# Kernel tuning notes

Hardware: AMD Instinct MI355X
Metric: run time of the kernel (lower is better)

Reference implementation:

```python
import jax, jax.numpy as jnp
import numpy as np

N = 50000
E = 400000
C = 64
H = 6  # heads, hardcoded in the module
NEG_SLOPE = 0.2
EPS = 1e-8


def setup_inputs() -> dict:
    key = jax.random.key(0)
    ks = jax.random.split(key, 10)
    x = jax.random.normal(ks[0], (N, C), dtype=jnp.float32)
    ei = jax.random.randint(ks[1], (2, E), 0, N)
    loop = jnp.arange(N)
    # forward() first calls add_remaining_self_loops -> GCN consumes edges + self loops
    src = jnp.concatenate([ei[0], loop])
    dst = jnp.concatenate([ei[1], loop])
    # gen_subs: subindex = self loops (i->i) plus reversed edges (t->i) for edge (i,t)
    sub_src = jnp.concatenate([loop, ei[1]])
    sub_dst = jnp.concatenate([loop, ei[0]])

    def glorot(k, shape):
        stdv = np.sqrt(6.0 / (shape[-2] + shape[-1]))
        return jax.random.uniform(k, shape, jnp.float32, -stdv, stdv)

    W_gcn = glorot(ks[2], (C, C))           # gnn_intra_cluster (GCNConv)
    b_gcn = jnp.zeros((C,), jnp.float32)
    weight = glorot(ks[3], (C, H * C))      # self.weight
    attention = glorot(ks[4], (1, H, 2 * C))  # self.attention
    W1 = glorot(ks[5], (C, C))              # simiConv.lin1 (no bias)
    W2 = glorot(ks[6], (C, 1))              # simiConv.lin2
    b2 = jnp.zeros((1,), jnp.float32)
    return {"x": x, "W_gcn": W_gcn, "b_gcn": b_gcn, "weight": weight,
            "attention": attention, "W1": W1, "W2": W2, "b2": b2,
            "src": src, "dst": dst, "sub_src": sub_src, "sub_dst": sub_dst}


def _gcn(x, W, b, src, dst, n):
    # PyG GCNConv's gcn_norm appends its own self loops on top of the ones
    # already added by forward()'s add_remaining_self_loops.
    loop = jnp.arange(n)
    s = jnp.concatenate([src, loop])
    d = jnp.concatenate([dst, loop])
    deg = jax.ops.segment_sum(jnp.ones_like(s, dtype=x.dtype), d, num_segments=n)
    dinv = jax.lax.rsqrt(jnp.maximum(deg, 1.0e-12))
    norm = dinv[s] * dinv[d]                      # [E']
    h = x @ W                                     # [N, C]
    out = jax.ops.segment_sum(h[s] * norm[:, None], d, num_segments=n)
    return out + b


def reference(x, W_gcn, b_gcn, weight, attention, W1, W2, b2,
              src, dst, sub_src, sub_dst):
    n = x.shape[0]
    # intra-cluster GCN
    xpj = _gcn(x, W_gcn, b_gcn, src, dst, n)      # [N, C]
    # multi-head attention pooling over subindex
    h = (xpj @ weight).reshape(n, H, C)           # [N, H, C]
    hi = h[sub_src]                               # [Es, H, C] (x_i in message)
    hmax = jax.ops.segment_max(hi, sub_dst, num_segments=n)  # [N, H, C]
    att_i = attention[:, :, :C]                   # [1, H, C]
    att_j = attention[:, :, C:]
    alpha = (hi * att_i).sum(-1) + (hmax[sub_dst] * att_j).sum(-1)  # [Es, H]
    alpha = jnp.where(alpha >= 0, alpha, NEG_SLOPE * alpha)
    # segment softmax over destination nodes (dropout p=0)
    amax = jax.ops.segment_max(alpha, sub_dst, num_segments=n)
    e = jnp.exp(alpha - amax[sub_dst])
    denom = jax.ops.segment_sum(e, sub_dst, num_segments=n)
    alpha = e / denom[sub_dst]
    xa = jax.ops.segment_sum(hi * alpha[:, :, None], sub_dst, num_segments=n)
    xm = xa.mean(axis=1)                          # [N, C]
    # simiConv score: message = x_cluster_i * cos(x_i, x_j), aggr='add'
    a = xm @ W1                                   # [N, C]
    bsc = xm @ W2 + b2                            # [N, 1]
    ai = a[sub_dst]
    aj = a[sub_src]
    cos = (ai * aj).sum(-1) / (jnp.maximum(jnp.linalg.norm(ai, axis=-1), EPS)
                               * jnp.maximum(jnp.linalg.norm(aj, axis=-1), EPS))
    score = jax.ops.segment_sum(bsc[sub_dst, 0] * cos, sub_dst, num_segments=n)
    fitness = jax.nn.sigmoid(score)               # [N]
    return fitness
```

## Files before the change

kernel.cpp:

```cpp
#include <hip/hip_runtime.h>
#include <math.h>

#define TPB 256
#define NEG_SLOPE 0.2f
#define COS_EPS 1e-8f
#define NH 6
#define GSTRIDE 68
#define DCACHE 12
#define SALS 8

__device__ inline float wave_sum64(float v) {
  #pragma unroll
  for (int off = 32; off > 0; off >>= 1) v += __shfl_down(v, off);
  return __shfl(v, 0);
}
__device__ inline float wave_max64(float v) {
  #pragma unroll
  for (int off = 32; off > 0; off >>= 1) v = fmaxf(v, __shfl_down(v, off));
  return __shfl(v, 0);
}
__device__ inline unsigned short f2bf(float f) {
  unsigned u = __float_as_uint(f);
  unsigned r = (u + 0x7fffu + ((u >> 16) & 1u)) >> 16;
  return (unsigned short)r;
}
__device__ inline float bf2f(unsigned short b) {
  return __uint_as_float(((unsigned)b) << 16);
}
__device__ inline unsigned packbf(float lo, float hi) {
  return (unsigned)f2bf(lo) | ((unsigned)f2bf(hi) << 16);
}
__device__ inline float bflo(unsigned u) { return __uint_as_float(u << 16); }
__device__ inline float bfhi(unsigned u) { return __uint_as_float(u & 0xffff0000u); }

#define GS_LOOP(i, total) \
  for (long i = (long)blockIdx.x * blockDim.x + threadIdx.x; i < (total); \
       i += (long)gridDim.x * blockDim.x)

__global__ void k_cnt(const int* __restrict__ src, const int* __restrict__ dst,
                      int* __restrict__ gcnt, int* __restrict__ scnt, long E) {
  GS_LOOP(e, E) {
    atomicAdd(&gcnt[dst[e]], 1);
    atomicAdd(&scnt[src[e]], 1);
  }
}

__global__ __launch_bounds__(1024)
void k_scanA(const int* __restrict__ gcnt, const int* __restrict__ scnt,
             int* __restrict__ bsum, float* __restrict__ dinv, int n, int nb) {
  const int b = blockIdx.x;
  const bool isS = b >= nb;
  const int tb = isS ? b - nb : b;
  const int* cnt = isS ? scnt : gcnt;
  const int t = threadIdx.x;
  const int i0 = tb * 2048 + 2 * t;
  int v0 = (i0 < n) ? cnt[i0] : 0;
  int v1 = (i0 + 1 < n) ? cnt[i0 + 1] : 0;
  if (!isS) {
    if (i0 < n)     dinv[i0]     = rsqrtf((float)v0 + 2.0f);
    if (i0 + 1 < n) dinv[i0 + 1] = rsqrtf((float)v1 + 2.0f);
  }
  __shared__ int red[16];
  int x = v0 + v1;
  #pragma unroll
  for (int o = 32; o > 0; o >>= 1) x += __shfl_down(x, o);
  const int lane = t & 63, wv = t >> 6;
  if (lane == 0) red[wv] = x;
  __syncthreads();
  if (t < 64) {
    int w = (t < 16) ? red[t] : 0;
    #pragma unroll
    for (int o = 32; o > 0; o >>= 1) w += __shfl_down(w, o);
    if (t == 0) bsum[b] = w;
  }
}

__global__ void k_scanB(int* __restrict__ bsum, int nb) {
  const int lane = threadIdx.x;
  if (nb <= 32) {
    int half = lane >> 5, idx = lane & 31;
    int base = half * nb;
    int v = (idx < nb) ? bsum[base + idx] : 0;
    int orig = v;
    #pragma unroll
    for (int d2 = 1; d2 < 32; d2 <<= 1) {
      int y = __shfl_up(v, d2, 32);
      if (idx >= d2) v += y;
    }
    if (idx < nb) bsum[base + idx] = v - orig;
  } else if (lane == 0) {
    int run = 0;
    for (int i = 0; i < nb; ++i) { int v = bsum[i]; bsum[i] = run; run += v; }
    run = 0;
    for (int i = 0; i < nb; ++i) { int v = bsum[nb + i]; bsum[nb + i] = run; run += v; }
  }
}

__global__ __launch_bounds__(1024)
void k_scanC(const int* __restrict__ gcnt, int* __restrict__ goff, int* __restrict__ gcur,
             const int* __restrict__ scnt, int* __restrict__ soff, int* __restrict__ scur,
             const int* __restrict__ bsum, int n, int nb) {
  const int b = blockIdx.x;
  const bool isS = b >= nb;
  const int tb = isS ? b - nb : b;
  const int* cnt = isS ? scnt : gcnt;
  int* off = isS ? soff : goff;
  int* cur = isS ? scur : gcur;
  const int t = threadIdx.x;
  const int i0 = tb * 2048 + 2 * t;
  int v0 = (i0 < n) ? cnt[i0] : 0;
  int v1 = (i0 + 1 < n) ? cnt[i0 + 1] : 0;
  int s2 = v0 + v1;
  const int lane = t & 63, wv = t >> 6;
  int x = s2;
  #pragma unroll
  for (int d2 = 1; d2 < 64; d2 <<= 1) {
    int y = __shfl_up(x, d2);
    if (lane >= d2) x += y;
  }
  __shared__ int wsum[16];
  if (lane == 63) wsum[wv] = x;
  __syncthreads();
  if (t < 64) {
    int w = (t < 16) ? wsum[t] : 0;
    #pragma unroll
    for (int d2 = 1; d2 < 16; d2 <<= 1) {
      int y = __shfl_up(w, d2);
      if ((int)t >= d2) w += y;
    }
    if (t < 16) wsum[t] = w;
  }
  __syncthreads();
  int ex = x - s2 + (wv ? wsum[wv - 1] : 0) + bsum[b];
  if (i0 < n)     { cur[i0] = ex;          off[i0 + 1] = ex + v0; }
  if (i0 + 1 < n) { cur[i0 + 1] = ex + v0; off[i0 + 2] = ex + v0 + v1; }
  if (i0 == 0) off[0] = 0;
}

__global__ void k_scatter(const int* __restrict__ src, const int* __restrict__ dst,
                          int* __restrict__ gcur, int* __restrict__ gcsr,
                          int* __restrict__ scur, int* __restrict__ scsr, long E) {
  GS_LOOP(e, E) {
    int s = src[e], d = dst[e];
    int p1 = atomicAdd(&gcur[d], 1); gcsr[p1] = s;
    int p2 = atomicAdd(&scur[s], 1); scsr[p2] = d;
  }
}

template <int MODE>
__global__ __launch_bounds__(256)
void k_gemm64v3(const float* __restrict__ A, const float* __restrict__ W,
                float* __restrict__ out32, unsigned short* __restrict__ out16,
                const float* __restrict__ rowscale,
                const float* __restrict__ W2, const float* __restrict__ b2,
                float* __restrict__ bsc, int n, int Mtot) {
  __shared__ float At[64 * GSTRIDE];
  __shared__ float Wl[64 * GSTRIDE];
  const int t  = threadIdx.x;
  const int tx = t & 15;
  const int ty = t >> 4;
  const int col0 = blockIdx.y * 64;
  const long row0 = (long)blockIdx.x * 64;

  #pragma unroll
  for (int i = 0; i < 4; ++i) {
    int k = ty + 16 * i;
    float4 wv = *(const float4*)&W[(long)k * Mtot + col0 + 4 * tx];
    *(float4*)&Wl[k * GSTRIDE + 4 * tx] = wv;
  }
  #pragma unroll
  for (int i = 0; i < 4; ++i) {
    int r = ty + 16 * i;
    long gr = row0 + r; if (gr >= n) gr = n - 1;
    float4 av = *(const float4*)&A[gr * 64 + 4 * tx];
    At[(4 * tx + 0) * GSTRIDE + r] = av.x;
    At[(4 * tx + 1) * GSTRIDE + r] = av.y;
    At[(4 * tx + 2) * GSTRIDE + r] = av.z;
    At[(4 * tx + 3) * GSTRIDE + r] = av.w;
  }
  __syncthreads();

  const int c0 = 4 * tx;
  const int r0 = 4 * ty;
  float acc[4][4] = {};
  #pragma unroll
  for (int k = 0; k < 64; ++k) {
    float4 av = *(const float4*)&At[k * GSTRIDE + r0];
    float4 wv = *(const float4*)&Wl[k * GSTRIDE + c0];
    acc[0][0] = fmaf(av.x, wv.x, acc[0][0]); acc[0][1] = fmaf(av.x, wv.y, acc[0][1]);
    acc[0][2] = fmaf(av.x, wv.z, acc[0][2]); acc[0][3] = fmaf(av.x, wv.w, acc[0][3]);
    acc[1][0] = fmaf(av.y, wv.x, acc[1][0]); acc[1][1] = fmaf(av.y, wv.y, acc[1][1]);
    acc[1][2] = fmaf(av.y, wv.z, acc[1][2]); acc[1][3] = fmaf(av.y, wv.w, acc[1][3]);
    acc[2][0] = fmaf(av.z, wv.x, acc[2][0]); acc[2][1] = fmaf(av.z, wv.y, acc[2][1]);
    acc[2][2] = fmaf(av.z, wv.z, acc[2][2]); acc[2][3] = fmaf(av.z, wv.w, acc[2][3]);
    acc[3][0] = fmaf(av.w, wv.x, acc[3][0]); acc[3][1] = fmaf(av.w, wv.y, acc[3][1]);
    acc[3][2] = fmaf(av.w, wv.z, acc[3][2]); acc[3][3] = fmaf(av.w, wv.w, acc[3][3]);
  }

  if constexpr (MODE == 0) {
    #pragma unroll
    for (int i = 0; i < 4; ++i) {
      long gr = row0 + r0 + i;
      if (gr < n)
        *(float4*)&out32[gr * Mtot + col0 + c0] =
          make_float4(acc[i][0], acc[i][1], acc[i][2], acc[i][3]);
    }
  }
  if constexpr (MODE == 1) {
    #pragma unroll
    for (int i = 0; i < 4; ++i) {
      long gr = row0 + r0 + i;
      if (gr < n) {
        float sc = rowscale[gr];
        ushort4 v;
        v.x = f2bf(acc[i][0] * sc); v.y = f2bf(acc[i][1] * sc);
        v.z = f2bf(acc[i][2] * sc); v.w = f2bf(acc[i][3] * sc);
        *(ushort4*)&out16[gr * 64 + c0] = v;
      }
    }
  }
  if constexpr (MODE == 2) {
    float p[4], q[4];
    #pragma unroll
    for (int i = 0; i < 4; ++i) {
      q[i] = acc[i][0]*acc[i][0] + acc[i][1]*acc[i][1] +
             acc[i][2]*acc[i][2] + acc[i][3]*acc[i][3];
      p[i] = At[(c0+0) * GSTRIDE + r0 + i] * W2[c0+0] +
             At[(c0+1) * GSTRIDE + r0 + i] * W2[c0+1] +
             At[(c0+2) * GSTRIDE + r0 + i] * W2[c0+2] +
             At[(c0+3) * GSTRIDE + r0 + i] * W2[c0+3];
    }
    #pragma unroll
    for (int m = 1; m < 16; m <<= 1) {
      #pragma unroll
      for (int i = 0; i < 4; ++i) { p[i] += __shfl_xor(p[i], m); q[i] += __shfl_xor(q[i], m); }
    }
    float bb = b2[0];
    #pragma unroll
    for (int i = 0; i < 4; ++i) {
      long gr = row0 + r0 + i;
      if (gr < n) {
        float rn = 1.0f / fmaxf(sqrtf(q[i]), COS_EPS);
        ushort4 v;
        v.x = f2bf(acc[i][0] * rn); v.y = f2bf(acc[i][1] * rn);
        v.z = f2bf(acc[i][2] * rn); v.w = f2bf(acc[i][3] * rn);
        *(ushort4*)&out16[gr * 64 + c0] = v;
        if (tx == 0) bsc[gr] = p[i] + bb;
      }
    }
  }
}

__global__ __launch_bounds__(256)
void k_gemm_h2(const float* __restrict__ A, const float* __restrict__ W,
               unsigned* __restrict__ h2p, const float* __restrict__ att,
               float* __restrict__ sal, int n) {
  __shared__ float At[64 * GSTRIDE];
  __shared__ float Wl[64 * GSTRIDE];
  const int t  = threadIdx.x;
  const int tx = t & 15;
  const int ty = t >> 4;
  const long row0 = (long)blockIdx.x * 64;
  const int c0 = 4 * tx;
  const int r0 = 4 * ty;

  #pragma unroll
  for (int i = 0; i < 4; ++i) {
    int r = ty + 16 * i;
    long gr = row0 + r; if (gr >= n) gr = n - 1;
    float4 av = *(const float4*)&A[gr * 64 + 4 * tx];
    At[(4 * tx + 0) * GSTRIDE + r] = av.x;
    At[(4 * tx + 1) * GSTRIDE + r] = av.y;
    At[(4 * tx + 2) * GSTRIDE + r] = av.z;
    At[(4 * tx + 3) * GSTRIDE + r] = av.w;
  }
  float4 wr[4];
  #pragma unroll
  for (int i = 0; i < 4; ++i)
    wr[i] = *(const float4*)&W[(long)(ty + 16 * i) * 384 + 4 * tx];

  float4 acc[6][4];
  #pragma unroll
  for (int h = 0; h < 6; ++h)
    #pragma unroll
    for (int i = 0; i < 4; ++i) acc[h][i] = make_float4(0.f, 0.f, 0.f, 0.f);

  #pragma unroll
  for (int head = 0; head < 6; ++head) {
    #pragma unroll
    for (int i = 0; i < 4; ++i)
      *(float4*)&Wl[(ty + 16 * i) * GSTRIDE + 4 * tx] = wr[i];
    __syncthreads();
    if (head < 5) {
      #pragma unroll
      for (int i = 0; i < 4; ++i)
        wr[i] = *(const float4*)&W[(long)(ty + 16 * i) * 384 + (head + 1) * 64 + 4 * tx];
    }
    #pragma unroll 16
    for (int k = 0; k < 64; ++k) {
      float4 av = *(const float4*)&At[k * GSTRIDE + r0];
      float4 wv = *(const float4*)&Wl[k * GSTRIDE + c0];
      acc[head][0].x = fmaf(av.x, wv.x, acc[head][0].x);
      acc[head][0].y = fmaf(av.x, wv.y, acc[head][0].y);
      acc[head][0].z = fmaf(av.x, wv.z, acc[head][0].z);
      acc[head][0].w = fmaf(av.x, wv.w, acc[head][0].w);
      acc[head][1].x = fmaf(av.y, wv.x, acc[head][1].x);
      acc[head][1].y = fmaf(av.y, wv.y, acc[head][1].y);
      acc[head][1].z = fmaf(av.y, wv.z, acc[head][1].z);
      acc[head][1].w = fmaf(av.y, wv.w, acc[head][1].w);
      acc[head][2].x = fmaf(av.z, wv.x, acc[head][2].x);
      acc[head][2].y = fmaf(av.z, wv.y, acc[head][2].y);
      acc[head][2].z = fmaf(av.z, wv.z, acc[head][2].z);
      acc[head][2].w = fmaf(av.z, wv.w, acc[head][2].w);
      acc[head][3].x = fmaf(av.w, wv.x, acc[head][3].x);
      acc[head][3].y = fmaf(av.w, wv.y, acc[head][3].y);
      acc[head][3].z = fmaf(av.w, wv.z, acc[head][3].z);
      acc[head][3].w = fmaf(av.w, wv.w, acc[head][3].w);
    }
    __syncthreads();
  }

  #pragma unroll
  for (int i = 0; i < 4; ++i) {
    long gr = row0 + r0 + i;
    if (gr < n) {
      uint4 u0, u1, u2;
      u0.x = packbf(acc[0][i].x, acc[1][i].x);
      u0.y = packbf(acc[2][i].x, acc[3][i].x);
      u0.z = packbf(acc[4][i].x, acc[5][i].x);
      u0.w = packbf(acc[0][i].y, acc[1][i].y);
      u1.x = packbf(acc[2][i].y, acc[3][i].y);
      u1.y = packbf(acc[4][i].y, acc[5][i].y);
      u1.z = packbf(acc[0][i].z, acc[1][i].z);
      u1.w = packbf(acc[2][i].z, acc[3][i].z);
      u2.x = packbf(acc[4][i].z, acc[5][i].z);
      u2.y = packbf(acc[0][i].w, acc[1][i].w);
      u2.z = packbf(acc[2][i].w, acc[3][i].w);
      u2.w = packbf(acc[4][i].w, acc[5][i].w);
      unsigned* dstp = &h2p[gr * 192 + c0 * 3];
      *(uint4*)(dstp + 0) = u0;
      *(uint4*)(dstp + 4) = u1;
      *(uint4*)(dstp + 8) = u2;
    }
  }
  #pragma unroll
  for (int head = 0; head < 6; ++head) {
    float a0 = att[head * 128 + c0 + 0], a1 = att[head * 128 + c0 + 1];
    float a2 = att[head * 128 + c0 + 2], a3 = att[head * 128 + c0 + 3];
    float p[4];
    #pragma unroll
    for (int i = 0; i < 4; ++i)
      p[i] = acc[head][i].x * a0 + acc[head][i].y * a1 +
             acc[head][i].z * a2 + acc[head][i].w * a3;
    #pragma unroll
    for (int m = 1; m < 16; m <<= 1) {
      #pragma unroll
      for (int i = 0; i < 4; ++i) p[i] += __shfl_xor(p[i], m);
    }
    if (tx == 0) {
      #pragma unroll
      for (int i = 0; i < 4; ++i) {
        long gr = row0 + r0 + i;
        if (gr < n) sal[gr * SALS + head] = p[i];
      }
    }
  }
}

__global__ __launch_bounds__(256)
void k_gcnb(const int* __restrict__ goff, const int* __restrict__ gcsr,
            const unsigned* __restrict__ hs32, const float* __restrict__ dinv,
            const float* __restrict__ bg, float* __restrict__ xpj, int n) {
  const int lane = threadIdx.x & 63;
  const int p = lane & 31;
  const int hf = lane >> 5;
  const int d = blockIdx.x * 4 + (threadIdx.x >> 6);
  if (d >= n) return;
  const int o0 = goff[d], o1 = goff[d + 1];
  float ax = 0.f, ay = 0.f;
  for (int j = o0 + hf; j < o1; j += 2) {
    long s = gcsr[j];
    unsigned u = hs32[s * 32 + p];
    ax += bflo(u); ay += bfhi(u);
  }
  ax += __shfl_xor(ax, 32);
  ay += __shfl_xor(ay, 32);
  if (hf == 0) {
    unsigned us = hs32[(long)d * 32 + p];
    float di = dinv[d];
    float2 bv = *(const float2*)&bg[2 * p];
    float2 r;
    r.x = bv.x + di * (ax + 2.0f * bflo(us));
    r.y = bv.y + di * (ay + 2.0f * bfhi(us));
    *(float2*)&xpj[(long)d * 64 + 2 * p] = r;
  }
}

__global__ __launch_bounds__(256)
void k_mega(const int* __restrict__ soff, const int* __restrict__ scsr,
            const unsigned* __restrict__ h2p, const float* __restrict__ sal,
            const float* __restrict__ att, float* __restrict__ xm, int n) {
  const int lane = threadIdx.x & 63;
  const int d = blockIdx.x * 4 + (threadIdx.x >> 6);
  if (d >= n) return;
  const int o0 = soff[d], o1 = soff[d + 1];
  const int deg = o1 - o0;
  const int td  = deg + 1;

  unsigned ck0[DCACHE], ck1[DCACHE], ck2[DCACHE];
  float hm[NH];
  {
    const unsigned* rp = &h2p[(long)d * 192 + lane * 3];
    unsigned u0 = rp[0], u1 = rp[1], u2 = rp[2];
    ck0[0] = u0; ck1[0] = u1; ck2[0] = u2;
    hm[0] = bflo(u0); hm[1] = bfhi(u0);
    hm[2] = bflo(u1); hm[3] = bfhi(u1);
    hm[4] = bflo(u2); hm[5] = bfhi(u2);
  }
  #pragma unroll
  for (int idx = 1; idx < DCACHE; ++idx) {
    unsigned u0 = 0, u1 = 0, u2 = 0;
    if (idx < td) {
      long s = scsr[o0 + idx - 1];
      const unsigned* rp = &h2p[s * 192 + lane * 3];
      u0 = rp[0]; u1 = rp[1]; u2 = rp[2];
      hm[0] = fmaxf(hm[0], bflo(u0)); hm[1] = fmaxf(hm[1], bfhi(u0));
      hm[2] = fmaxf(hm[2], bflo(u1)); hm[3] = fmaxf(hm[3], bfhi(u1));
      hm[4] = fmaxf(hm[4], bflo(u2)); hm[5] = fmaxf(hm[5], bfhi(u2));
    }
    ck0[idx] = u0; ck1[idx] = u1; ck2[idx] = u2;
  }
  for (int j = o0 + DCACHE - 1; j < o1; ++j) {
    long s = scsr[j];
    const unsigned* rp = &h2p[s * 192 + lane * 3];
    unsigned u0 = rp[0], u1 = rp[1], u2 = rp[2];
    hm[0] = fmaxf(hm[0], bflo(u0)); hm[1] = fmaxf(hm[1], bfhi(u0));
    hm[2] = fmaxf(hm[2], bflo(u1)); hm[3] = fmaxf(hm[3], bfhi(u1));
    hm[4] = fmaxf(hm[4], bflo(u2)); hm[5] = fmaxf(hm[5], bfhi(u2));
  }

  float dal[NH];
  #pragma unroll
  for (int h = 0; h < NH; ++h)
    dal[h] = wave_sum64(hm[h] * att[h * 128 + 64 + lane]);

  float acc[NH], den[NH];
  #pragma unroll
  for (int h = 0; h < NH; ++h) acc[h] = 0.f;

  if (td <= 64) {
    const bool act = lane < td;
    float4 sA = make_float4(0, 0, 0, 0), sB = sA;
    if (act) {
      int sE = (lane == 0) ? d : scsr[o0 + lane - 1];
      const float4* sp = (const float4*)&sal[(long)sE * SALS];
      sA = sp[0]; sB = sp[1];
    }
    float svv[NH] = {sA.x, sA.y, sA.z, sA.w, sB.x, sB.y};
    float e6[NH];
    #pragma unroll
    for (int h = 0; h < NH; ++h) {
      float al = svv[h] + dal[h];
      al = (al >= 0.f) ? al : NEG_SLOPE * al;
      float a = act ? al : -INFINITY;
      float mx = wave_max64(a);
      e6[h] = act ? expf(a - mx) : 0.f;
      den[h] = wave_sum64(e6[h]);
    }
    #pragma unroll
    for (int idx = 0; idx < DCACHE; ++idx) {
      if (idx < td) {
        float w0 = __shfl(e6[0], idx), w1 = __shfl(e6[1], idx);
        float w2 = __shfl(e6[2], idx), w3 = __shfl(e6[3], idx);
        float w4 = __shfl(e6[4], idx), w5 = __shfl(e6[5], idx);
        acc[0] = fmaf(bflo(ck0[idx]), w0, acc[0]);
        acc[1] = fmaf(bfhi(ck0[idx]), w1, acc[1]);
        acc[2] = fmaf(bflo(ck1[idx]), w2, acc[2]);
        acc[3] = fmaf(bfhi(ck1[idx]), w3, acc[3]);
        acc[4] = fmaf(bflo(ck2[idx]), w4, acc[4]);
        acc[5] = fmaf(bfhi(ck2[idx]), w5, acc[5]);
      }
    }
    for (int j = o0 + DCACHE - 1; j < o1; ++j) {
      int ii = j - o0 + 1;
      long s = scsr[j];
      const unsigned* rp = &h2p[s * 192 + lane * 3];
      unsigned u0 = rp[0], u1 = rp[1], u2 = rp[2];
      float w0 = __shfl(e6[0], ii), w1 = __shfl(e6[1], ii);
      float w2 = __shfl(e6[2], ii), w3 = __shfl(e6[3], ii);
      float w4 = __shfl(e6[4], ii), w5 = __shfl(e6[5], ii);
      acc[0] = fmaf(bflo(u0), w0, acc[0]);
      acc[1] = fmaf(bfhi(u0), w1, acc[1]);
      acc[2] = fmaf(bflo(u1), w2, acc[2]);
      acc[3] = fmaf(bfhi(u1), w3, acc[3]);
      acc[4] = fmaf(bflo(u2), w4, acc[4]);
      acc[5] = fmaf(bfhi(u2), w5, acc[5]);
    }
  } else {
    float asf[NH];
    {
      const float4* sp = (const float4*)&sal[(long)d * SALS];
      float4 sA = sp[0], sB = sp[1];
      float svv[NH] = {sA.x, sA.y, sA.z, sA.w, sB.x, sB.y};
      #pragma unroll
      for (int h = 0; h < NH; ++h) {
        float al = svv[h] + dal[h];
        asf[h] = (al >= 0.f) ? al : NEG_SLOPE * al;
      }
    }
    float mx[NH];
    #pragma unroll
    for (int h = 0; h < NH; ++h) mx[h] = asf[h];
    for (int base = o0; base < o1; base += 64) {
      int j = base + lane;
      float a6[NH];
      if (j < o1) {
        long s = scsr[j];
        const float4* sp = (const float4*)&sal[s * SALS];
        float4 sA = sp[0], sB = sp[1];
        float svv[NH] = {sA.x, sA.y, sA.z, sA.w, sB.x, sB.y};
        #pragma unroll
        for (int h = 0; h < NH; ++h) {
          float al = svv[h] + dal[h];
          a6[h] = (al >= 0.f) ? al : NEG_SLOPE * al;
        }
      } else {
        #pragma unroll
        for (int h = 0; h < NH; ++h) a6[h] = -INFINITY;
      }
      #pragma unroll
      for (int h = 0; h < NH; ++h) mx[h] = fmaxf(mx[h], wave_max64(a6[h]));
    }
    #pragma unroll
    for (int h = 0; h < NH; ++h) {
      float es = expf(asf[h] - mx[h]);
      den[h] = es;
    }
    acc[0] = bflo(ck0[0]) * den[0]; acc[1] = bfhi(ck0[0]) * den[1];
    acc[2] = bflo(ck1[0]) * den[2]; acc[3] = bfhi(ck1[0]) * den[3];
    acc[4] = bflo(ck2[0]) * den[4]; acc[5] = bfhi(ck2[0]) * den[5];
    for (int base = o0; base < o1; base += 64) {
      int cs = o1 - base; if (cs > 64) cs = 64;
      int j = base + lane;
      float e6[NH]; int s = 0;
      if (j < o1) {
        s = scsr[j];
        const float4* sp = (const float4*)&sal[(long)s * SALS];
        float4 sA = sp[0], sB = sp[1];
        float svv[NH] = {sA.x, sA.y, sA.z, sA.w, sB.x, sB.y};
        #pragma unroll
        for (int h = 0; h < NH; ++h) {
          float al = svv[h] + dal[h];
          al = (al >= 0.f) ? al : NEG_SLOPE * al;
          e6[h] = expf(al - mx[h]);
        }
      } else {
        #pragma unroll
        for (int h = 0; h < NH; ++h) e6[h] = 0.f;
      }
      #pragma unroll
      for (int h = 0; h < NH; ++h) den[h] += wave_sum64(e6[h]);
      for (int jj = 0; jj < cs; ++jj) {
        int sj = __shfl(s, jj);
        const unsigned* rp = &h2p[(long)sj * 192 + lane * 3];
        unsigned u0 = rp[0], u1 = rp[1], u2 = rp[2];
        float w0 = __shfl(e6[0], jj), w1 = __shfl(e6[1], jj);
        float w2 = __shfl(e6[2], jj), w3 = __shfl(e6[3], jj);
        float w4 = __shfl(e6[4], jj), w5 = __shfl(e6[5], jj);
        acc[0] = fmaf(bflo(u0), w0, acc[0]);
        acc[1] = fmaf(bfhi(u0), w1, acc[1]);
        acc[2] = fmaf(bflo(u1), w2, acc[2]);
        acc[3] = fmaf(bfhi(u1), w3, acc[3]);
        acc[4] = fmaf(bflo(u2), w4, acc[4]);
        acc[5] = fmaf(bfhi(u2), w5, acc[5]);
      }
    }
  }

  float o = 0.f;
  #pragma unroll
  for (int h = 0; h < NH; ++h) o += acc[h] / den[h];
  xm[(long)d * 64 + lane] = o * (1.0f / NH);
}

__global__ __launch_bounds__(256)
void k_cosout(const int* __restrict__ soff, const int* __restrict__ scsr,
              const unsigned* __restrict__ an32, const float* __restrict__ bsc,
              float* __restrict__ out, int n) {
  const int lane = threadIdx.x & 63;
  const int p = lane & 31;
  const int hf = lane >> 5;
  const int d = blockIdx.x * 4 + (threadIdx.x >> 6);
  if (d >= n) return;
  const int o0 = soff[d], o1 = soff[d + 1];
  unsigned ud = an32[(long)d * 32 + p];
  float adx = bflo(ud), ady = bfhi(ud);
  float cl = 0.f;
  for (int j = o0 + hf; j < o1; j += 2) {
    long s = scsr[j];
    unsigned u = an32[s * 32 + p];
    cl += adx * bflo(u) + ady * bfhi(u);
  }
  float cs = wave_sum64(cl) + 1.0f;
  if (lane == 0) out[d] = 1.0f / (1.0f + expf(-bsc[d] * cs));
}

static inline unsigned gsblocks(long total) {
  long b = (total + TPB - 1) / TPB;
  if (b > 131072) b = 131072;
  return (unsigned)b;
}

extern "C" void kernel_launch(void* const* d_in, const int* in_sizes, int n_in,
                              void* d_out, int out_size, void* d_ws, size_t ws_size,
                              hipStream_t stream) {
  const float* x   = (const float*)d_in[0];
  const float* Wg  = (const float*)d_in[1];
  const float* bg  = (const float*)d_in[2];
  const float* Wt  = (const float*)d_in[3];
  const float* att = (const float*)d_in[4];
  const float* W1  = (const float*)d_in[5];
  const float* W2  = (const float*)d_in[6];
  const float* b2  = (const float*)d_in[7];
  const int* src   = (const int*)d_in[8];
  const int* dst   = (const int*)d_in[9];

  const long n   = in_sizes[0] / 64;
  const long en  = in_sizes[8];
  const long E   = en - n;
  const int  nb  = (int)((n + 2047) / 2048);

  char* base = (char*)d_ws;
  size_t off = 0;
  auto alloc = [&](size_t bytes) -> void* {
    void* p = base + off;
    off += (bytes + 255) & ~(size_t)255;
    return p;
  };
  int*   gcnt = (int*)alloc(n * 4);
  int*   scnt = (int*)alloc(n * 4);
  int*   goff = (int*)alloc((n + 1) * 4);
  int*   soff = (int*)alloc((n + 1) * 4);
  int*   gcur = (int*)alloc(n * 4);
  int*   scur = (int*)alloc(n * 4);
  int*   gcsr = (int*)alloc(E * 4);
  int*   scsr = (int*)alloc(E * 4);
  int*   bsum = (int*)alloc(2 * (size_t)nb * 4);
  float* dinv = (float*)alloc(n * 4);
  unsigned* hs32 = (unsigned*)alloc(n * 32 * 4);
  float* xpj  = (float*)alloc(n * 64 * 4);
  float* xmb  = (float*)alloc(n * 64 * 4);
  unsigned* h2p = (unsigned*)alloc(n * 192 * 4);
  float* sal  = (float*)alloc(n * SALS * 4);
  float* bsc  = (float*)alloc(n * 4);
  unsigned short* anorm = (unsigned short*)xpj;
  float* out  = (float*)d_out;

  const unsigned rowblk  = (unsigned)((n + 63) / 64);
  const unsigned nodeblk = (unsigned)((n + 3) / 4);

  hipMemsetAsync(gcnt, 0, (size_t)((char*)scnt - (char*)gcnt) + n * 4, stream);
  k_cnt<<<gsblocks(E), TPB, 0, stream>>>(src, dst, gcnt, scnt, E);
  k_scanA<<<2 * nb, 1024, 0, stream>>>(gcnt, scnt, bsum, dinv, (int)n, nb);
  k_scanB<<<1, 64, 0, stream>>>(bsum, nb);
  k_scanC<<<2 * nb, 1024, 0, stream>>>(gcnt, goff, gcur, scnt, soff, scur,
                                       bsum, (int)n, nb);
  k_scatter<<<gsblocks(E), TPB, 0, stream>>>(src, dst, gcur, gcsr, scur, scsr, E);

  { dim3 g(rowblk, 1);
    k_gemm64v3<1><<<g, 256, 0, stream>>>(x, Wg, nullptr, (unsigned short*)hs32,
                                         dinv, nullptr, nullptr, nullptr, (int)n, 64); }

  k_gcnb<<<nodeblk, 256, 0, stream>>>(goff, gcsr, hs32, dinv, bg, xpj, (int)n);

  k_gemm_h2<<<rowblk, 256, 0, stream>>>(xpj, Wt, h2p, att, sal, (int)n);

  k_mega<<<nodeblk, 256, 0, stream>>>(soff, scsr, h2p, sal, att, xmb, (int)n);

  { dim3 g(rowblk, 1);
    k_gemm64v3<2><<<g, 256, 0, stream>>>(xmb, W1, nullptr, anorm, nullptr,
                                         W2, b2, bsc, (int)n, 64); }

  k_cosout<<<nodeblk, 256, 0, stream>>>(soff, scsr, (const unsigned*)anorm,
                                        bsc, out, (int)n);
}
```

Measured before the change: 369.8 us.

## Replace softmax max pass with analytic bound, fold block-prefix scan into scanC

The segment softmax no longer runs a separate max-reduction pass over neighbours. It subtracts a per-head shift K = max(dal, 0) instead, which removes one gather pass over sal and the wave max reductions. The separate k_scanB launch is dropped, and each scanC block now sums the preceding block totals itself with a wave reduction. DCACHE rises from 12 to 16, and the unused MODE 0 GEMM epilogue is removed. The shift is not a true maximum, so exp can overflow or underflow if the source-side attention logits are large, which trades numerical safety for one fewer pass.

```diff
diff --git a/kernel.cpp b/kernel.cpp
--- a/kernel.cpp
+++ b/kernel.cpp
@@ -6,7 +6,7 @@
 #define COS_EPS 1e-8f
 #define NH 6
 #define GSTRIDE 68
-#define DCACHE 12
+#define DCACHE 16
 #define SALS 8
 
 __device__ inline float wave_sum64(float v) {
@@ -14,10 +14,10 @@
   for (int off = 32; off > 0; off >>= 1) v += __shfl_down(v, off);
   return __shfl(v, 0);
 }
-__device__ inline float wave_max64(float v) {
-  #pragma unroll
-  for (int off = 32; off > 0; off >>= 1) v = fmaxf(v, __shfl_down(v, off));
-  return __shfl(v, 0);
+__device__ inline int wave_isum64(int v) {
+  #pragma unroll
+  for (int off = 32; off > 0; off >>= 1) v += __shfl_down(v, off);
+  return v;
 }
 __device__ inline unsigned short f2bf(float f) {
   unsigned u = __float_as_uint(f);
@@ -75,27 +75,6 @@
   }
 }
 
-__global__ void k_scanB(int* __restrict__ bsum, int nb) {
-  const int lane = threadIdx.x;
-  if (nb <= 32) {
-    int half = lane >> 5, idx = lane & 31;
-    int base = half * nb;
-    int v = (idx < nb) ? bsum[base + idx] : 0;
-    int orig = v;
-    #pragma unroll
-    for (int d2 = 1; d2 < 32; d2 <<= 1) {
-      int y = __shfl_up(v, d2, 32);
-      if (idx >= d2) v += y;
-    }
-    if (idx < nb) bsum[base + idx] = v - orig;
-  } else if (lane == 0) {
-    int run = 0;
-    for (int i = 0; i < nb; ++i) { int v = bsum[i]; bsum[i] = run; run += v; }
-    run = 0;
-    for (int i = 0; i < nb; ++i) { int v = bsum[nb + i]; bsum[nb + i] = run; run += v; }
-  }
-}
-
 __global__ __launch_bounds__(1024)
 void k_scanC(const int* __restrict__ gcnt, int* __restrict__ goff, int* __restrict__ gcur,
              const int* __restrict__ scnt, int* __restrict__ soff, int* __restrict__ scur,
@@ -107,6 +86,14 @@
   int* off = isS ? soff : goff;
   int* cur = isS ? scur : gcur;
   const int t = threadIdx.x;
+
+  __shared__ int pfx_s;
+  if (t < 64) {
+    int v = (t < tb) ? bsum[(isS ? nb : 0) + t] : 0;
+    v = wave_isum64(v);
+    if (t == 0) pfx_s = v;
+  }
+
   const int i0 = tb * 2048 + 2 * t;
   int v0 = (i0 < n) ? cnt[i0] : 0;
   int v1 = (i0 + 1 < n) ? cnt[i0 + 1] : 0;
@@ -131,7 +118,7 @@
     if (t < 16) wsum[t] = w;
   }
   __syncthreads();
-  int ex = x - s2 + (wv ? wsum[wv - 1] : 0) + bsum[b];
+  int ex = x - s2 + (wv ? wsum[wv - 1] : 0) + pfx_s;
   if (i0 < n)     { cur[i0] = ex;          off[i0 + 1] = ex + v0; }
   if (i0 + 1 < n) { cur[i0 + 1] = ex + v0; off[i0 + 2] = ex + v0 + v1; }
   if (i0 == 0) off[0] = 0;
@@ -197,15 +184,6 @@
     acc[3][2] = fmaf(av.w, wv.z, acc[3][2]); acc[3][3] = fmaf(av.w, wv.w, acc[3][3]);
   }
 
-  if constexpr (MODE == 0) {
-    #pragma unroll
-    for (int i = 0; i < 4; ++i) {
-      long gr = row0 + r0 + i;
-      if (gr < n)
-        *(float4*)&out32[gr * Mtot + col0 + c0] =
-          make_float4(acc[i][0], acc[i][1], acc[i][2], acc[i][3]);
-    }
-  }
   if constexpr (MODE == 1) {
     #pragma unroll
     for (int i = 0; i < 4; ++i) {
@@ -439,10 +417,12 @@
     hm[4] = fmaxf(hm[4], bflo(u2)); hm[5] = fmaxf(hm[5], bfhi(u2));
   }
 
-  float dal[NH];
-  #pragma unroll
-  for (int h = 0; h < NH; ++h)
+  float dal[NH], K[NH];
+  #pragma unroll
+  for (int h = 0; h < NH; ++h) {
     dal[h] = wave_sum64(hm[h] * att[h * 128 + 64 + lane]);
+    K[h] = fmaxf(dal[h], 0.f);
+  }
 
   float acc[NH], den[NH];
   #pragma unroll
@@ -462,9 +442,7 @@
     for (int h = 0; h < NH; ++h) {
       float al = svv[h] + dal[h];
       al = (al >= 0.f) ? al : NEG_SLOPE * al;
-      float a = act ? al : -INFINITY;
-      float mx = wave_max64(a);
-      e6[h] = act ? expf(a - mx) : 0.f;
+      e6[h] = act ? expf(al - K[h]) : 0.f;
       den[h] = wave_sum64(e6[h]);
     }
     #pragma unroll
@@ -497,7 +475,6 @@
       acc[5] = fmaf(bfhi(u2), w5, acc[5]);
     }
   } else {
-    float asf[NH];
     {
       const float4* sp = (const float4*)&sal[(long)d * SALS];
       float4 sA = sp[0], sB = sp[1];
@@ -505,36 +482,10 @@
       #pragma unroll
       for (int h = 0; h < NH; ++h) {
         float al = svv[h] + dal[h];
-        asf[h] = (al >= 0.f) ? al : NEG_SLOPE * al;
+        al = (al >= 0.f) ? al : NEG_SLOPE * al;
+        float es = expf(al - K[h]);
+        den[h] = es;
       }
-    }
-    float mx[NH];
-    #pragma unroll
-    for (int h = 0; h < NH; ++h) mx[h] = asf[h];
-    for (int base = o0; base < o1; base += 64) {
-      int j = base + lane;
-      float a6[NH];
-      if (j < o1) {
-        long s = scsr[j];
-        const float4* sp = (const float4*)&sal[s * SALS];
-        float4 sA = sp[0], sB = sp[1];
-        float svv[NH] = {sA.x, sA.y, sA.z, sA.w, sB.x, sB.y};
-        #pragma unroll
-        for (int h = 0; h < NH; ++h) {
-          float al = svv[h] + dal[h];
-          a6[h] = (al >= 0.f) ? al : NEG_SLOPE * al;
-        }
-      } else {
-        #pragma unroll
-        for (int h = 0; h < NH; ++h) a6[h] = -INFINITY;
-      }
-      #pragma unroll
-      for (int h = 0; h < NH; ++h) mx[h] = fmaxf(mx[h], wave_max64(a6[h]));
-    }
-    #pragma unroll
-    for (int h = 0; h < NH; ++h) {
-      float es = expf(asf[h] - mx[h]);
-      den[h] = es;
     }
     acc[0] = bflo(ck0[0]) * den[0]; acc[1] = bfhi(ck0[0]) * den[1];
     acc[2] = bflo(ck1[0]) * den[2]; acc[3] = bfhi(ck1[0]) * den[3];
@@ -552,7 +503,7 @@
         for (int h = 0; h < NH; ++h) {
           float al = svv[h] + dal[h];
           al = (al >= 0.f) ? al : NEG_SLOPE * al;
-          e6[h] = expf(al - mx[h]);
+          e6[h] = expf(al - K[h]);
         }
       } else {
         #pragma unroll
@@ -662,7 +613,6 @@
   hipMemsetAsync(gcnt, 0, (size_t)((char*)scnt - (char*)gcnt) + n * 4, stream);
   k_cnt<<<gsblocks(E), TPB, 0, stream>>>(src, dst, gcnt, scnt, E);
   k_scanA<<<2 * nb, 1024, 0, stream>>>(gcnt, scnt, bsum, dinv, (int)n, nb);
-  k_scanB<<<1, 64, 0, stream>>>(bsum, nb);
   k_scanC<<<2 * nb, 1024, 0, stream>>>(gcnt, goff, gcur, scnt, soff, scur,
                                        bsum, (int)n, nb);
   k_scatter<<<gsblocks(E), TPB, 0, stream>>>(src, dst, gcur, gcsr, scur, scsr, E);
```

Result: no change. 370.2 us (+0.1%).
